# Optimization experiments

Measured on AMD Instinct MI355X. Metric: run time of the kernel, lower is better.

Reference implementation:

```python
import jax, jax.numpy as jnp
import numpy as np

N = 512        # n_t (sequence length of observations)
D_IN = 128     # input feature dim
PROJ = 128     # proj_dim
ENC = 128      # enc_dim
H = 4          # num_head
E = PROJ // H  # per-head dim = 32
SCALE = 1.0 / np.float32(np.sqrt(E))


def setup_inputs() -> dict:
    key = jax.random.key(0)
    ks = jax.random.split(key, 14)
    g = lambda k, sh: (jax.random.normal(k, sh, jnp.float32) * 0.05)
    inp = jax.random.normal(ks[0], (N, D_IN), jnp.float32)
    # irregular observation times, sorted ascending
    pos = jnp.sort(jax.random.uniform(ks[1], (N,), jnp.float32) * 100.0)
    # PosEncodingBlock frequency vector f: exp(arange(0,enc,2) * -(ln(10000)/enc))
    f = jnp.exp(jnp.arange(0, ENC, 2, dtype=jnp.float32) * (-(np.log(10000.0) / ENC)))
    return {
        "inp": inp, "pos": pos, "f": f,
        "Wq": g(ks[2], (D_IN, PROJ)), "bq": g(ks[3], (PROJ,)),
        "Wk": g(ks[4], (D_IN, PROJ)), "bk": g(ks[5], (PROJ,)),
        "Wv": g(ks[6], (D_IN, PROJ)), "bv": g(ks[7], (PROJ,)),
        "Wqt": g(ks[8], (D_IN, PROJ)), "bqt": g(ks[9], (PROJ,)),
        "Wt": g(ks[10], (ENC, PROJ)), "bt": g(ks[11], (PROJ,)),
    }


def _heads(x):
    # 'n (h e) -> h n e'
    return x.reshape(N, H, E).transpose(1, 0, 2)


def reference(inp, pos, f, Wq, bq, Wk, bk, Wv, bv, Wqt, bqt, Wt, bt):
    q = _heads(inp @ Wq + bq)   # (h, n, e)
    k = _heads(inp @ Wk + bk)
    v = _heads(inp @ Wv + bv)
    qt = _heads(inp @ Wqt + bqt)

    score = jnp.einsum('hne,hme->hnm', q, k) * SCALE  # (h, n, n)

    # Equivariant relative-time positional encoding: (n, n, ENC)
    rel_time = pos[:, None] - pos[None, :]                    # (n, n)
    angles = rel_time[..., None] * f                          # (n, n, ENC/2)
    # rearrange([sin, cos], 'z t l k -> t l (k z)') interleaves sin/cos per freq
    pos_enc = jnp.stack([jnp.sin(angles), jnp.cos(angles)], axis=-1).reshape(N, N, ENC)

    # time_dense then 'n1 n2 (h e) -> h n1 n2 e'
    t = (pos_enc @ Wt + bt).reshape(N, N, H, E).transpose(2, 0, 1, 3)  # (h, n, n, e)
    # tf.linalg.matvec(t, q_t): bias[h,i,j] = sum_e t[h,i,j,e] * qt[h,i,e]
    score = score + jnp.einsum('hnme,hne->hnm', t, qt) * SCALE

    mask = jnp.tril(jnp.ones((N, N), dtype=bool))
    score = jnp.where(mask, score, -jnp.inf)
    weight = jax.nn.softmax(score, axis=-1)
    weight = jnp.where(mask, weight, 0.0)
    # dropout is identity at inference

    out = jnp.einsum('hnm,hme->hne', weight, v)  # (h, n, e)
    return out.transpose(1, 0, 2).reshape(N, PROJ)  # 'h n e -> n (h e)'
```

## Files before the change

kernel.cpp:

```cpp
#include <hip/hip_runtime.h>
#include <math.h>

namespace {
constexpr int N = 512;
constexpr int DIN = 128;
constexpr int PROJ = 128;
constexpr int H = 4;
constexpr int E = 32;
constexpr int KF = 64;
constexpr int FEAT = E + 2*KF;
constexpr float SCALE = 0.17677669529663687f;
constexpr int TI = 8;
constexpr int JQ = 8;
constexpr int CHUNK = 64;
}

__device__ __forceinline__ float wave_max(float v) {
  #pragma unroll
  for (int o = 32; o > 0; o >>= 1) v = fmaxf(v, __shfl_xor(v, o, 64));
  return v;
}
__device__ __forceinline__ float wave_sum(float v) {
  #pragma unroll
  for (int o = 32; o > 0; o >>= 1) v += __shfl_xor(v, o, 64);
  return v;
}

__global__ __launch_bounds__(256)
void proj_feat_kernel(const float* __restrict__ inp,
                      const float* __restrict__ pos, const float* __restrict__ f,
                      const float* __restrict__ Wq, const float* __restrict__ bq,
                      const float* __restrict__ Wk, const float* __restrict__ bk,
                      const float* __restrict__ Wv, const float* __restrict__ bv,
                      const float* __restrict__ Wqt, const float* __restrict__ bqt,
                      const float* __restrict__ Wt, const float* __restrict__ bt,
                      float* __restrict__ Afeat, float* __restrict__ BTk,
                      float* __restrict__ Vmat, float* __restrict__ Btrig,
                      float* __restrict__ c0)
{
  const int bx = blockIdx.x;
  const int t = threadIdx.x;
  const int rowTile = bx & 127, mat = bx >> 7;
  const int i0 = rowTile * 4;
  const int c = t & 127, half = t >> 7;

  __shared__ float x[4][DIN];
  __shared__ float qt_l[4][PROJ];
  __shared__ float ss[4][KF], sc[4][KF];
  __shared__ float ul[4][H][PROJ];

  #pragma unroll
  for (int r = 0; r < 2; ++r) {
    const int id = t + r * 256;
    x[id >> 7][id & 127] = inp[i0 * DIN + id];
  }
  const float* W; const float* bvec;
  switch (mat) {
    case 0:  W = Wq;  bvec = bq;  break;
    case 1:  W = Wk;  bvec = bk;  break;
    case 2:  W = Wv;  bvec = bv;  break;
    default: W = Wqt; bvec = bqt; break;
  }
  __syncthreads();

  const int r0 = half * 2, r1 = r0 + 1;
  float a0 = 0.f, a1 = 0.f;
  #pragma unroll 8
  for (int d = 0; d < DIN; d += 2) {
    const float w0 = W[d * PROJ + c];
    const float w1 = W[(d + 1) * PROJ + c];
    const float2 x0 = *(const float2*)&x[r0][d];
    const float2 x1 = *(const float2*)&x[r1][d];
    a0 += w0 * x0.x + w1 * x0.y;
    a1 += w0 * x1.x + w1 * x1.y;
  }
  const float bb = bvec[c];
  a0 += bb; a1 += bb;
  const int h = c >> 5, e = c & 31;
  const int row0 = i0 + r0, row1 = i0 + r1;
  if (mat == 0) {
    Afeat[(h * N + row0) * FEAT + e] = a0;
    Afeat[(h * N + row1) * FEAT + e] = a1;
    return;
  } else if (mat == 1) {
    BTk[(size_t)(h * E + e) * N + row0] = a0;
    BTk[(size_t)(h * E + e) * N + row1] = a1;
    return;
  } else if (mat == 2) {
    Vmat[(h * N + row0) * E + e] = a0;
    Vmat[(h * N + row1) * E + e] = a1;
    return;
  }
  qt_l[r0][c] = a0;
  qt_l[r1][c] = a1;
  {
    const int r = t >> 6, k = t & 63;
    float s_, c_;
    sincosf(pos[i0 + r] * f[k], &s_, &c_);
    ss[r][k] = s_; sc[r][k] = c_;
  }
  __syncthreads();

  {
    const int g = t >> 7;
    const float* wrow = &Wt[c * PROJ];
    #pragma unroll
    for (int hh = 0; hh < H; ++hh) {
      float uA = 0.f, uB = 0.f;
      #pragma unroll
      for (int e4 = 0; e4 < E; e4 += 4) {
        const float4 w = *(const float4*)&wrow[hh * E + e4];
        const float4 qA = *(const float4*)&qt_l[2 * g][hh * E + e4];
        const float4 qB = *(const float4*)&qt_l[2 * g + 1][hh * E + e4];
        uA += w.x * qA.x + w.y * qA.y + w.z * qA.z + w.w * qA.w;
        uB += w.x * qB.x + w.y * qB.y + w.z * qB.z + w.w * qB.w;
      }
      ul[2 * g][hh][c] = uA;
      ul[2 * g + 1][hh][c] = uB;
    }
  }
  if (t < 16) {
    const int r = t >> 2, hh = t & 3;
    float acc = 0.f;
    for (int e2 = 0; e2 < E; ++e2) acc += bt[hh * E + e2] * qt_l[r][hh * E + e2];
    c0[hh * N + i0 + r] = acc;
  }
  __syncthreads();

  {
    const int k = t & 63, hh = t >> 6;
    #pragma unroll
    for (int r = 0; r < 4; ++r) {
      const float u0 = ul[r][hh][2 * k], u1 = ul[r][hh][2 * k + 1];
      const float s_ = ss[r][k], c_ = sc[r][k];
      Afeat[(hh * N + i0 + r) * FEAT + E + k]      =  u0 * s_ + u1 * c_;
      Afeat[(hh * N + i0 + r) * FEAT + E + KF + k] = -u0 * c_ + u1 * s_;
      if (hh == 0) {
        Btrig[k * N + i0 + r]        = c_;
        Btrig[(KF + k) * N + i0 + r] = s_;
      }
    }
  }
}

__global__ __launch_bounds__(256)
void attn_partial(const float* __restrict__ Afeat, const float* __restrict__ BTk,
                  const float* __restrict__ Btrig, const float* __restrict__ Vmat,
                  const float* __restrict__ c0,
                  float* __restrict__ Po, float* __restrict__ Pm,
                  float* __restrict__ Ps)
{
  const int b = blockIdx.x, h = blockIdx.y, q = blockIdx.z;
  const int i0 = b * TI, jbase = q * CHUNK;
  if (jbase > i0) return;
  const int t = threadIdx.x;
  const int lane = t & 63;
  const int rh = __builtin_amdgcn_readfirstlane(t >> 6);
  const int j = jbase + lane;

  __shared__ float pT[CHUNK][12];
  __shared__ float obuf[16][TI][32];

  const float* A0 = Afeat + (size_t)(h * N + i0 + rh * 2) * FEAT;
  const float* A1 = A0 + FEAT;
  const float cc0 = c0[h * N + i0 + rh * 2];
  const float cc1 = c0[h * N + i0 + rh * 2 + 1];

  float acc0 = 0.f, acc1 = 0.f;
  {
    const float* Bp = BTk + (size_t)h * E * N + j;
    #pragma unroll
    for (int d = 0; d < E; d += 4) {
      const float b0 = Bp[(size_t)(d + 0) * N];
      const float b1 = Bp[(size_t)(d + 1) * N];
      const float b2 = Bp[(size_t)(d + 2) * N];
      const float b3 = Bp[(size_t)(d + 3) * N];
      const float4 a0 = *(const float4*)&A0[d];
      const float4 a1 = *(const float4*)&A1[d];
      acc0 += a0.x * b0 + a0.y * b1 + a0.z * b2 + a0.w * b3;
      acc1 += a1.x * b0 + a1.y * b1 + a1.z * b2 + a1.w * b3;
    }
  }
  {
    const float* Bp = Btrig + j;
    #pragma unroll 8
    for (int d = 0; d < 2 * KF; d += 4) {
      const float b0 = Bp[(size_t)(d + 0) * N];
      const float b1 = Bp[(size_t)(d + 1) * N];
      const float b2 = Bp[(size_t)(d + 2) * N];
      const float b3 = Bp[(size_t)(d + 3) * N];
      const float4 a0 = *(const float4*)&A0[E + d];
      const float4 a1 = *(const float4*)&A1[E + d];
      acc0 += a0.x * b0 + a0.y * b1 + a0.z * b2 + a0.w * b3;
      acc1 += a1.x * b0 + a1.y * b1 + a1.z * b2 + a1.w * b3;
    }
  }

  const int i_0 = i0 + rh * 2, i_1 = i_0 + 1;
  const float s0 = (j <= i_0) ? (acc0 + cc0) * SCALE : -INFINITY;
  const float s1 = (j <= i_1) ? (acc1 + cc1) * SCALE : -INFINITY;

  const float m0 = wave_max(s0);
  const float m1 = wave_max(s1);
  const float p0 = __expf(s0 - m0);
  const float p1 = __expf(s1 - m1);
  const float sum0 = wave_sum(p0);
  const float sum1 = wave_sum(p1);

  *(float2*)&pT[lane][rh * 2] = make_float2(p0, p1);
  if (lane == 0) {
    const int base = (h * N + i_0) * JQ + q;
    Pm[base]      = m0; Ps[base]      = sum0;
    Pm[base + JQ] = m1; Ps[base + JQ] = sum1;
  }
  __syncthreads();

  const int e2 = (t & 15) * 2, gg = t >> 4;
  float2 o[TI];
  #pragma unroll
  for (int r = 0; r < TI; ++r) o[r] = make_float2(0.f, 0.f);
  const float* Vh = Vmat + ((size_t)h * N + jbase) * E + e2;
  #pragma unroll
  for (int it = 0; it < CHUNK / 16; ++it) {
    const int jl = gg + 16 * it;
    const float2 vv = *(const float2*)&Vh[jl * E];
    const float4 pa = *(const float4*)&pT[jl][0];
    const float4 pb = *(const float4*)&pT[jl][4];
    o[0].x += pa.x * vv.x; o[0].y += pa.x * vv.y;
    o[1].x += pa.y * vv.x; o[1].y += pa.y * vv.y;
    o[2].x += pa.z * vv.x; o[2].y += pa.z * vv.y;
    o[3].x += pa.w * vv.x; o[3].y += pa.w * vv.y;
    o[4].x += pb.x * vv.x; o[4].y += pb.x * vv.y;
    o[5].x += pb.y * vv.x; o[5].y += pb.y * vv.y;
    o[6].x += pb.z * vv.x; o[6].y += pb.z * vv.y;
    o[7].x += pb.w * vv.x; o[7].y += pb.w * vv.y;
  }
  #pragma unroll
  for (int r = 0; r < TI; ++r) *(float2*)&obuf[gg][r][e2] = o[r];
  __syncthreads();
  {
    const int r = t >> 5, e = t & 31;
    float tot = 0.f;
    #pragma unroll
    for (int g2 = 0; g2 < 16; ++g2) tot += obuf[g2][r][e];
    Po[((size_t)(h * N + i0 + r) * JQ + q) * E + e] = tot;
  }
}

__global__ __launch_bounds__(256)
void attn_combine(const float* __restrict__ Po, const float* __restrict__ Pm,
                  const float* __restrict__ Ps, float* __restrict__ out)
{
  const int gid = blockIdx.x * 256 + threadIdx.x;
  const int task = gid >> 5, e = gid & 31;
  const int h = task >> 9, i = task & (N - 1);
  const int nq = (i >> 6) + 1;
  float m = -INFINITY;
  for (int qq = 0; qq < nq; ++qq) m = fmaxf(m, Pm[task * JQ + qq]);
  float s = 0.f, o = 0.f;
  for (int qq = 0; qq < nq; ++qq) {
    const float w = __expf(Pm[task * JQ + qq] - m);
    s += Ps[task * JQ + qq] * w;
    o += Po[(size_t)(task * JQ + qq) * E + e] * w;
  }
  out[i * PROJ + h * E + e] = o / s;
}

extern "C" void kernel_launch(void* const* d_in, const int* in_sizes, int n_in,
                              void* d_out, int out_size, void* d_ws, size_t ws_size,
                              hipStream_t stream) {
  const float* inp = (const float*)d_in[0];
  const float* pos = (const float*)d_in[1];
  const float* f   = (const float*)d_in[2];
  const float* Wq  = (const float*)d_in[3];
  const float* bq  = (const float*)d_in[4];
  const float* Wk  = (const float*)d_in[5];
  const float* bk  = (const float*)d_in[6];
  const float* Wv  = (const float*)d_in[7];
  const float* bv  = (const float*)d_in[8];
  const float* Wqt = (const float*)d_in[9];
  const float* bqt = (const float*)d_in[10];
  const float* Wt  = (const float*)d_in[11];
  const float* bt  = (const float*)d_in[12];
  float* out = (float*)d_out;

  float* ws    = (float*)d_ws;
  float* Afeat = ws;
  float* BTk   = Afeat + H * N * FEAT;
  float* Btrig = BTk + (size_t)H * E * N;
  float* Vmat  = Btrig + 2 * KF * N;
  float* c0    = Vmat + H * N * E;
  float* Po    = c0 + H * N;
  float* Pm    = Po + (size_t)H * N * JQ * E;
  float* Ps    = Pm + H * N * JQ;

  proj_feat_kernel<<<512, 256, 0, stream>>>(inp, pos, f, Wq, bq, Wk, bk, Wv, bv,
                                            Wqt, bqt, Wt, bt,
                                            Afeat, BTk, Vmat, Btrig, c0);
  attn_partial<<<dim3(N / TI, H, JQ), 256, 0, stream>>>(Afeat, BTk, Btrig, Vmat,
                                                        c0, Po, Pm, Ps);
  attn_combine<<<H * N * E / 256, 256, 0, stream>>>(Po, Pm, Ps, out);
}
```

Before: 30.27 us.

## Double key chunk per attention block and split qt/time-feature blocks finer

Attention partial blocks now cover 128 keys instead of 64, with each lane computing two adjacent keys via float2 loads. This halves the number of split partials and the combine work, and reuses the A-row loads across two keys. The projection kernel gives the qt/time-feature path its own 256 blocks of 2 rows each, so that heavy path is spread over more blocks. Shared-memory padding is changed to reduce bank conflicts. The trade-off is fewer attention blocks, coarser causal skipping and more registers per thread.

```diff
diff --git a/kernel.cpp b/kernel.cpp
--- a/kernel.cpp
+++ b/kernel.cpp
@@ -11,8 +11,8 @@
 constexpr int FEAT = E + 2*KF;
 constexpr float SCALE = 0.17677669529663687f;
 constexpr int TI = 8;
-constexpr int JQ = 8;
-constexpr int CHUNK = 64;
+constexpr int JQ = 4;
+constexpr int CHUNK = 128;
 }
 
 __device__ __forceinline__ float wave_max(float v) {
@@ -40,64 +40,79 @@
 {
   const int bx = blockIdx.x;
   const int t = threadIdx.x;
-  const int rowTile = bx & 127, mat = bx >> 7;
-  const int i0 = rowTile * 4;
-  const int c = t & 127, half = t >> 7;
-
-  __shared__ float x[4][DIN];
-  __shared__ float qt_l[4][PROJ];
-  __shared__ float ss[4][KF], sc[4][KF];
-  __shared__ float ul[4][H][PROJ];
-
-  #pragma unroll
-  for (int r = 0; r < 2; ++r) {
-    const int id = t + r * 256;
-    x[id >> 7][id & 127] = inp[i0 * DIN + id];
-  }
-  const float* W; const float* bvec;
-  switch (mat) {
-    case 0:  W = Wq;  bvec = bq;  break;
-    case 1:  W = Wk;  bvec = bk;  break;
-    case 2:  W = Wv;  bvec = bv;  break;
-    default: W = Wqt; bvec = bqt; break;
-  }
-  __syncthreads();
-
-  const int r0 = half * 2, r1 = r0 + 1;
-  float a0 = 0.f, a1 = 0.f;
-  #pragma unroll 8
-  for (int d = 0; d < DIN; d += 2) {
-    const float w0 = W[d * PROJ + c];
-    const float w1 = W[(d + 1) * PROJ + c];
-    const float2 x0 = *(const float2*)&x[r0][d];
-    const float2 x1 = *(const float2*)&x[r1][d];
-    a0 += w0 * x0.x + w1 * x0.y;
-    a1 += w0 * x1.x + w1 * x1.y;
-  }
-  const float bb = bvec[c];
-  a0 += bb; a1 += bb;
-  const int h = c >> 5, e = c & 31;
-  const int row0 = i0 + r0, row1 = i0 + r1;
-  if (mat == 0) {
-    Afeat[(h * N + row0) * FEAT + e] = a0;
-    Afeat[(h * N + row1) * FEAT + e] = a1;
+  const int c = t & 127;
+
+  if (bx < 384) {
+    const int mat = bx >> 7, rowTile = bx & 127;
+    const int i0 = rowTile * 4;
+    const int half = t >> 7;
+    __shared__ float x[4][DIN];
+    #pragma unroll
+    for (int r = 0; r < 2; ++r) {
+      const int id = t + r * 256;
+      x[id >> 7][id & 127] = inp[i0 * DIN + id];
+    }
+    const float* W; const float* bvec;
+    switch (mat) {
+      case 0:  W = Wq; bvec = bq; break;
+      case 1:  W = Wk; bvec = bk; break;
+      default: W = Wv; bvec = bv; break;
+    }
+    __syncthreads();
+    const int r0 = half * 2, r1 = r0 + 1;
+    float a0 = 0.f, a1 = 0.f;
+    #pragma unroll 8
+    for (int d = 0; d < DIN; d += 2) {
+      const float w0 = W[d * PROJ + c];
+      const float w1 = W[(d + 1) * PROJ + c];
+      const float2 x0 = *(const float2*)&x[r0][d];
+      const float2 x1 = *(const float2*)&x[r1][d];
+      a0 += w0 * x0.x + w1 * x0.y;
+      a1 += w0 * x1.x + w1 * x1.y;
+    }
+    const float bb = bvec[c];
+    a0 += bb; a1 += bb;
+    const int h = c >> 5, e = c & 31;
+    const int row0 = i0 + r0, row1 = i0 + r1;
+    if (mat == 0) {
+      Afeat[(h * N + row0) * FEAT + e] = a0;
+      Afeat[(h * N + row1) * FEAT + e] = a1;
+    } else if (mat == 1) {
+      BTk[(size_t)(h * E + e) * N + row0] = a0;
+      BTk[(size_t)(h * E + e) * N + row1] = a1;
+    } else {
+      Vmat[(h * N + row0) * E + e] = a0;
+      Vmat[(h * N + row1) * E + e] = a1;
+    }
     return;
-  } else if (mat == 1) {
-    BTk[(size_t)(h * E + e) * N + row0] = a0;
-    BTk[(size_t)(h * E + e) * N + row1] = a1;
-    return;
-  } else if (mat == 2) {
-    Vmat[(h * N + row0) * E + e] = a0;
-    Vmat[(h * N + row1) * E + e] = a1;
-    return;
-  }
-  qt_l[r0][c] = a0;
-  qt_l[r1][c] = a1;
-  {
-    const int r = t >> 6, k = t & 63;
+  }
+
+  const int i0 = (bx - 384) * 2;
+  const int r = t >> 7;
+  __shared__ float x[2][DIN];
+  __shared__ float qt_l[2][PROJ];
+  __shared__ float ss[2][KF], sc[2][KF];
+  __shared__ float ul[2][H][PROJ];
+
+  x[r][c] = inp[i0 * DIN + t];
+  if (t < 128) {
+    const int rr = t >> 6, k = t & 63;
     float s_, c_;
-    sincosf(pos[i0 + r] * f[k], &s_, &c_);
-    ss[r][k] = s_; sc[r][k] = c_;
+    sincosf(pos[i0 + rr] * f[k], &s_, &c_);
+    ss[rr][k] = s_; sc[rr][k] = c_;
+  }
+  __syncthreads();
+
+  {
+    float a = 0.f;
+    #pragma unroll 8
+    for (int d = 0; d < DIN; d += 2) {
+      const float w0 = Wqt[d * PROJ + c];
+      const float w1 = Wqt[(d + 1) * PROJ + c];
+      const float2 xv = *(const float2*)&x[r][d];
+      a += w0 * xv.x + w1 * xv.y;
+    }
+    qt_l[r][c] = a + bqt[c];
   }
   __syncthreads();
 
@@ -105,39 +120,39 @@
     const int g = t >> 7;
     const float* wrow = &Wt[c * PROJ];
     #pragma unroll
-    for (int hh = 0; hh < H; ++hh) {
+    for (int hh = 2 * g; hh < 2 * g + 2; ++hh) {
       float uA = 0.f, uB = 0.f;
       #pragma unroll
       for (int e4 = 0; e4 < E; e4 += 4) {
         const float4 w = *(const float4*)&wrow[hh * E + e4];
-        const float4 qA = *(const float4*)&qt_l[2 * g][hh * E + e4];
-        const float4 qB = *(const float4*)&qt_l[2 * g + 1][hh * E + e4];
+        const float4 qA = *(const float4*)&qt_l[0][hh * E + e4];
+        const float4 qB = *(const float4*)&qt_l[1][hh * E + e4];
         uA += w.x * qA.x + w.y * qA.y + w.z * qA.z + w.w * qA.w;
         uB += w.x * qB.x + w.y * qB.y + w.z * qB.z + w.w * qB.w;
       }
-      ul[2 * g][hh][c] = uA;
-      ul[2 * g + 1][hh][c] = uB;
-    }
-  }
-  if (t < 16) {
-    const int r = t >> 2, hh = t & 3;
+      ul[0][hh][c] = uA;
+      ul[1][hh][c] = uB;
+    }
+  }
+  if (t < 8) {
+    const int rr = t & 1, hh = t >> 1;
     float acc = 0.f;
-    for (int e2 = 0; e2 < E; ++e2) acc += bt[hh * E + e2] * qt_l[r][hh * E + e2];
-    c0[hh * N + i0 + r] = acc;
+    for (int e2 = 0; e2 < E; ++e2) acc += bt[hh * E + e2] * qt_l[rr][hh * E + e2];
+    c0[hh * N + i0 + rr] = acc;
   }
   __syncthreads();
 
   {
     const int k = t & 63, hh = t >> 6;
     #pragma unroll
-    for (int r = 0; r < 4; ++r) {
-      const float u0 = ul[r][hh][2 * k], u1 = ul[r][hh][2 * k + 1];
-      const float s_ = ss[r][k], c_ = sc[r][k];
-      Afeat[(hh * N + i0 + r) * FEAT + E + k]      =  u0 * s_ + u1 * c_;
-      Afeat[(hh * N + i0 + r) * FEAT + E + KF + k] = -u0 * c_ + u1 * s_;
+    for (int rr = 0; rr < 2; ++rr) {
+      const float u0 = ul[rr][hh][2 * k], u1 = ul[rr][hh][2 * k + 1];
+      const float s_ = ss[rr][k], c_ = sc[rr][k];
+      Afeat[(hh * N + i0 + rr) * FEAT + E + k]      =  u0 * s_ + u1 * c_;
+      Afeat[(hh * N + i0 + rr) * FEAT + E + KF + k] = -u0 * c_ + u1 * s_;
       if (hh == 0) {
-        Btrig[k * N + i0 + r]        = c_;
-        Btrig[(KF + k) * N + i0 + r] = s_;
+        Btrig[k * N + i0 + rr]        = c_;
+        Btrig[(KF + k) * N + i0 + rr] = s_;
       }
     }
   }
@@ -156,58 +171,65 @@
   const int t = threadIdx.x;
   const int lane = t & 63;
   const int rh = __builtin_amdgcn_readfirstlane(t >> 6);
-  const int j = jbase + lane;
-
-  __shared__ float pT[CHUNK][12];
-  __shared__ float obuf[16][TI][32];
+  const int j0 = jbase + 2 * lane, j1 = j0 + 1;
+
+  __shared__ float pT[CHUNK][13];
+  __shared__ float obuf[16][TI][34];
 
   const float* A0 = Afeat + (size_t)(h * N + i0 + rh * 2) * FEAT;
   const float* A1 = A0 + FEAT;
   const float cc0 = c0[h * N + i0 + rh * 2];
   const float cc1 = c0[h * N + i0 + rh * 2 + 1];
 
-  float acc0 = 0.f, acc1 = 0.f;
-  {
-    const float* Bp = BTk + (size_t)h * E * N + j;
+  float acc00 = 0.f, acc01 = 0.f, acc10 = 0.f, acc11 = 0.f;
+  {
+    const float* Bp = BTk + (size_t)h * E * N + j0;
     #pragma unroll
     for (int d = 0; d < E; d += 4) {
-      const float b0 = Bp[(size_t)(d + 0) * N];
-      const float b1 = Bp[(size_t)(d + 1) * N];
-      const float b2 = Bp[(size_t)(d + 2) * N];
-      const float b3 = Bp[(size_t)(d + 3) * N];
+      const float2 b0 = *(const float2*)&Bp[(size_t)(d + 0) * N];
+      const float2 b1 = *(const float2*)&Bp[(size_t)(d + 1) * N];
+      const float2 b2 = *(const float2*)&Bp[(size_t)(d + 2) * N];
+      const float2 b3 = *(const float2*)&Bp[(size_t)(d + 3) * N];
       const float4 a0 = *(const float4*)&A0[d];
       const float4 a1 = *(const float4*)&A1[d];
-      acc0 += a0.x * b0 + a0.y * b1 + a0.z * b2 + a0.w * b3;
-      acc1 += a1.x * b0 + a1.y * b1 + a1.z * b2 + a1.w * b3;
-    }
-  }
-  {
-    const float* Bp = Btrig + j;
+      acc00 += a0.x * b0.x + a0.y * b1.x + a0.z * b2.x + a0.w * b3.x;
+      acc01 += a0.x * b0.y + a0.y * b1.y + a0.z * b2.y + a0.w * b3.y;
+      acc10 += a1.x * b0.x + a1.y * b1.x + a1.z * b2.x + a1.w * b3.x;
+      acc11 += a1.x * b0.y + a1.y * b1.y + a1.z * b2.y + a1.w * b3.y;
+    }
+  }
+  {
+    const float* Bp = Btrig + j0;
     #pragma unroll 8
     for (int d = 0; d < 2 * KF; d += 4) {
-      const float b0 = Bp[(size_t)(d + 0) * N];
-      const float b1 = Bp[(size_t)(d + 1) * N];
-      const float b2 = Bp[(size_t)(d + 2) * N];
-      const float b3 = Bp[(size_t)(d + 3) * N];
+      const float2 b0 = *(const float2*)&Bp[(size_t)(d + 0) * N];
+      const float2 b1 = *(const float2*)&Bp[(size_t)(d + 1) * N];
+      const float2 b2 = *(const float2*)&Bp[(size_t)(d + 2) * N];
+      const float2 b3 = *(const float2*)&Bp[(size_t)(d + 3) * N];
       const float4 a0 = *(const float4*)&A0[E + d];
       const float4 a1 = *(const float4*)&A1[E + d];
-      acc0 += a0.x * b0 + a0.y * b1 + a0.z * b2 + a0.w * b3;
-      acc1 += a1.x * b0 + a1.y * b1 + a1.z * b2 + a1.w * b3;
+      acc00 += a0.x * b0.x + a0.y * b1.x + a0.z * b2.x + a0.w * b3.x;
+      acc01 += a0.x * b0.y + a0.y * b1.y + a0.z * b2.y + a0.w * b3.y;
+      acc10 += a1.x * b0.x + a1.y * b1.x + a1.z * b2.x + a1.w * b3.x;
+      acc11 += a1.x * b0.y + a1.y * b1.y + a1.z * b2.y + a1.w * b3.y;
     }
   }
 
   const int i_0 = i0 + rh * 2, i_1 = i_0 + 1;
-  const float s0 = (j <= i_0) ? (acc0 + cc0) * SCALE : -INFINITY;
-  const float s1 = (j <= i_1) ? (acc1 + cc1) * SCALE : -INFINITY;
-
-  const float m0 = wave_max(s0);
-  const float m1 = wave_max(s1);
-  const float p0 = __expf(s0 - m0);
-  const float p1 = __expf(s1 - m1);
-  const float sum0 = wave_sum(p0);
-  const float sum1 = wave_sum(p1);
-
-  *(float2*)&pT[lane][rh * 2] = make_float2(p0, p1);
+  const float s00 = (j0 <= i_0) ? (acc00 + cc0) * SCALE : -INFINITY;
+  const float s01 = (j1 <= i_0) ? (acc01 + cc0) * SCALE : -INFINITY;
+  const float s10 = (j0 <= i_1) ? (acc10 + cc1) * SCALE : -INFINITY;
+  const float s11 = (j1 <= i_1) ? (acc11 + cc1) * SCALE : -INFINITY;
+
+  const float m0 = wave_max(fmaxf(s00, s01));
+  const float m1 = wave_max(fmaxf(s10, s11));
+  const float p00 = __expf(s00 - m0), p01 = __expf(s01 - m0);
+  const float p10 = __expf(s10 - m1), p11 = __expf(s11 - m1);
+  const float sum0 = wave_sum(p00 + p01);
+  const float sum1 = wave_sum(p10 + p11);
+
+  *(float2*)&pT[2 * lane    ][rh * 2] = make_float2(p00, p10);
+  *(float2*)&pT[2 * lane + 1][rh * 2] = make_float2(p01, p11);
   if (lane == 0) {
     const int base = (h * N + i_0) * JQ + q;
     Pm[base]      = m0; Ps[base]      = sum0;
@@ -254,7 +276,7 @@
   const int gid = blockIdx.x * 256 + threadIdx.x;
   const int task = gid >> 5, e = gid & 31;
   const int h = task >> 9, i = task & (N - 1);
-  const int nq = (i >> 6) + 1;
+  const int nq = (i >> 7) + 1;
   float m = -INFINITY;
   for (int qq = 0; qq < nq; ++qq) m = fmaxf(m, Pm[task * JQ + qq]);
   float s = 0.f, o = 0.f;
@@ -294,7 +316,7 @@
   float* Pm    = Po + (size_t)H * N * JQ * E;
   float* Ps    = Pm + H * N * JQ;
 
-  proj_feat_kernel<<<512, 256, 0, stream>>>(inp, pos, f, Wq, bq, Wk, bk, Wv, bv,
+  proj_feat_kernel<<<640, 256, 0, stream>>>(inp, pos, f, Wq, bq, Wk, bk, Wv, bv,
                                             Wqt, bqt, Wt, bt,
                                             Afeat, BTk, Vmat, Btrig, c0);
   attn_partial<<<dim3(N / TI, H, JQ), 256, 0, stream>>>(Afeat, BTk, Btrig, Vmat,
```

Result: slower. 37.48 us (+23.8%).
